# Performance work log

Measured on AMD Instinct MI355X. Metric: run time of the kernel, lower is better.

## Reference

```python
import jax, jax.numpy as jnp
import numpy as np

N_ATOMS = 100000
N_EDGES = 300000
ATOM_DIM = 32
BOND_DIM = 16
STEPS = 4


def setup_inputs() -> dict:
    key = jax.random.key(0)
    ks = jax.random.split(key, 8)
    atom_features = jax.random.normal(ks[0], (N_ATOMS, ATOM_DIM), dtype=jnp.float32)
    bond_features = jax.random.normal(ks[1], (N_EDGES, BOND_DIM), dtype=jnp.float32)
    pair_indices = jax.random.randint(ks[2], (N_EDGES, 2), 0, N_ATOMS, dtype=jnp.int64 if jax.config.jax_enable_x64 else jnp.int32)
    W_bond = jax.random.normal(ks[3], (BOND_DIM, ATOM_DIM * ATOM_DIM), dtype=jnp.float32) * 0.05
    b_bond = jnp.zeros((ATOM_DIM * ATOM_DIM,), dtype=jnp.float32)
    W_ih = jax.random.normal(ks[4], (3 * ATOM_DIM, ATOM_DIM), dtype=jnp.float32) * 0.1
    W_hh = jax.random.normal(ks[5], (3 * ATOM_DIM, ATOM_DIM), dtype=jnp.float32) * 0.1
    b_ih = jnp.zeros((3 * ATOM_DIM,), dtype=jnp.float32)
    b_hh = jnp.zeros((3 * ATOM_DIM,), dtype=jnp.float32)
    return {
        'atom_features': atom_features,
        'bond_features': bond_features,
        'pair_indices': pair_indices,
        'W_bond': W_bond, 'b_bond': b_bond,
        'W_ih': W_ih, 'W_hh': W_hh, 'b_ih': b_ih, 'b_hh': b_hh,
    }


def _gru_cell(x, h, W_ih, W_hh, b_ih, b_hh):
    # torch.nn.GRUCell semantics
    gi = x @ W_ih.T + b_ih  # [N, 3H]
    gh = h @ W_hh.T + b_hh
    i_r, i_z, i_n = jnp.split(gi, 3, axis=-1)
    h_r, h_z, h_n = jnp.split(gh, 3, axis=-1)
    r = jax.nn.sigmoid(i_r + h_r)
    z = jax.nn.sigmoid(i_z + h_z)
    n = jnp.tanh(i_n + r * h_n)
    return (1.0 - z) * n + z * h


def reference(atom_features, bond_features, pair_indices, W_bond, b_bond, W_ih, W_hh, b_ih, b_hh):
    n_atoms, d = atom_features.shape
    # Edge transform matrices (identical every step in the original; hoisted)
    edge_mats = (bond_features @ W_bond + b_bond).reshape(-1, d, d)  # [E, d, d]
    dst = pair_indices[:, 0]
    nbr = pair_indices[:, 1]
    h = atom_features
    for _ in range(STEPS):
        # gather neighbor states, per-edge matvec, scatter-add
        msg = jnp.einsum('eij,ej->ei', edge_mats, h[nbr])  # [E, d]
        agg = jax.ops.segment_sum(msg, dst, num_segments=n_atoms)  # [N, d]
        h = _gru_cell(agg, h, W_ih, W_hh, b_ih, b_hh)
    return h
```

## Files before the change

kernel.cpp:

```cpp
#include <hip/hip_runtime.h>
#include <hip/hip_cooperative_groups.h>

namespace cg = cooperative_groups;

#define NA 100000
#define NE 300000
#define STEPS 4
#define NTILES (NE / 16)
#define ATILES (NA / 16)

typedef _Float16 f16;
typedef _Float16 half8 __attribute__((ext_vector_type(8)));
using f32x4 = __attribute__((ext_vector_type(4))) float;

__global__ __launch_bounds__(256) void setup_kernel(
    const float* __restrict__ atom,
    const float* __restrict__ Wb, const float* __restrict__ bb,
    const float* __restrict__ Wih, const float* __restrict__ Whh,
    f16* __restrict__ hbf, f16* __restrict__ Wbt,
    f16* __restrict__ Wihb, f16* __restrict__ Whhb,
    int* __restrict__ rowcnt, int* __restrict__ total)
{
    int t = blockIdx.x * 256 + threadIdx.x;
    const int NH8 = NA * 32 / 8;
    if (t < NH8) {
        float4 a = reinterpret_cast<const float4*>(atom)[2 * t];
        float4 b = reinterpret_cast<const float4*>(atom)[2 * t + 1];
        half8 o;
        o[0]=(f16)a.x; o[1]=(f16)a.y; o[2]=(f16)a.z; o[3]=(f16)a.w;
        o[4]=(f16)b.x; o[5]=(f16)b.y; o[6]=(f16)b.z; o[7]=(f16)b.w;
        reinterpret_cast<half8*>(hbf)[t] = o;
        return;
    }
    int u = t - NH8;
    if (u < NA) {
        rowcnt[u] = 0;
        if (u == 0) *total = 0;
        return;
    }
    int v = u - NA;
    if (v < 17 * 32 * 32) {
        int j = v & 31, i = (v >> 5) & 31, k = v >> 10;
        float val = (k < 16) ? Wb[k * 1024 + i * 32 + j] : bb[i * 32 + j];
        int row = ((i & 4) ? 16 : 0) + ((i >> 3) << 2) + (i & 3);
        Wbt[(k * 32 + row) * 32 + j] = (f16)val;
    } else if (v < 17 * 32 * 32 + 3072) {
        int q = v - 17 * 32 * 32;
        Wihb[q] = (f16)Wih[q];
    } else if (v < 17 * 32 * 32 + 6144) {
        int q = v - 17 * 32 * 32 - 3072;
        Whhb[q] = (f16)Whh[q];
    }
}

__global__ __launch_bounds__(256) void hist_kernel(
    const int* __restrict__ pair, int* __restrict__ cnt)
{
    int e = blockIdx.x * 256 + threadIdx.x;
    if (e < NE) atomicAdd(&cnt[reinterpret_cast<const int2*>(pair)[e].x], 1);
}

__global__ __launch_bounds__(1024) void alloc_kernel(
    const int* __restrict__ cnt, int* __restrict__ start,
    int* __restrict__ next, int* __restrict__ total)
{
    __shared__ int tmp[1024];
    __shared__ int base;
    int g = blockIdx.x * 1024 + threadIdx.x;
    int v = (g < NA) ? cnt[g] : 0;
    tmp[threadIdx.x] = v;
    __syncthreads();
    for (int off = 1; off < 1024; off <<= 1) {
        int u = (threadIdx.x >= off) ? tmp[threadIdx.x - off] : 0;
        __syncthreads();
        tmp[threadIdx.x] += u;
        __syncthreads();
    }
    if (threadIdx.x == 1023) base = atomicAdd(total, tmp[1023]);
    __syncthreads();
    if (g < NA) {
        int s = base + tmp[threadIdx.x] - v;
        start[g] = s;
        next[g] = s;
    }
}

__global__ __launch_bounds__(256) void scatter_kernel(
    const float* __restrict__ bond, const int* __restrict__ pair,
    int* __restrict__ next, int* __restrict__ nbrp, f16* __restrict__ bondp)
{
    int e = blockIdx.x * 256 + threadIdx.x;
    if (e >= NE) return;
    int2 p = reinterpret_cast<const int2*>(pair)[e];
    int pos = atomicAdd(&next[p.x], 1);
    nbrp[pos] = p.y;
    const float4* b4 = reinterpret_cast<const float4*>(bond + (size_t)e * 16);
    float4 b0 = b4[0], b1 = b4[1], b2 = b4[2], b3 = b4[3];
    half8 o0, o1;
    o0[0]=(f16)b0.x; o0[1]=(f16)b0.y; o0[2]=(f16)b0.z; o0[3]=(f16)b0.w;
    o0[4]=(f16)b1.x; o0[5]=(f16)b1.y; o0[6]=(f16)b1.z; o0[7]=(f16)b1.w;
    o1[0]=(f16)b2.x; o1[1]=(f16)b2.y; o1[2]=(f16)b2.z; o1[3]=(f16)b2.w;
    o1[4]=(f16)b3.x; o1[5]=(f16)b3.y; o1[6]=(f16)b3.z; o1[7]=(f16)b3.w;
    half8* dst = reinterpret_cast<half8*>(bondp + (size_t)pos * 16);
    dst[0] = o0; dst[1] = o1;
}

__device__ __forceinline__ void msg_body(
    const f16* __restrict__ h, const f16* __restrict__ bondp,
    const int* __restrict__ nbrp, const f16* __restrict__ Wbt,
    f16* __restrict__ msgb, int wid, int nw, int col, int kg)
{
    half8 w0[17], w1[17];
#pragma unroll
    for (int t = 0; t < 17; ++t) {
        w0[t] = *reinterpret_cast<const half8*>(Wbt + (t * 32 + col) * 32 + kg * 8);
        w1[t] = *reinterpret_cast<const half8*>(Wbt + (t * 32 + 16 + col) * 32 + kg * 8);
    }
    int tile = wid;
    int pos = 0;
    half8 hf{}, cA{}, cB{};
    if (tile < NTILES) {
        pos = tile * 16 + col;
        int nbr0 = nbrp[pos];
        cA = *reinterpret_cast<const half8*>(bondp + (size_t)pos * 16);
        cB = *reinterpret_cast<const half8*>(bondp + (size_t)pos * 16 + 8);
        hf = *reinterpret_cast<const half8*>(h + (size_t)nbr0 * 32 + kg * 8);
    }
    while (tile < NTILES) {
        int tile2 = tile + nw;
        int pos2 = 0;
        half8 hf2{}, cA2{}, cB2{};
        if (tile2 < NTILES) {
            pos2 = tile2 * 16 + col;
            int nbr2 = nbrp[pos2];
            cA2 = *reinterpret_cast<const half8*>(bondp + (size_t)pos2 * 16);
            cB2 = *reinterpret_cast<const half8*>(bondp + (size_t)pos2 * 16 + 8);
            hf2 = *reinterpret_cast<const half8*>(h + (size_t)nbr2 * 32 + kg * 8);
        }
        f32x4 acc0 = {0.f, 0.f, 0.f, 0.f};
        f32x4 acc1 = {0.f, 0.f, 0.f, 0.f};
#pragma unroll
        for (int t = 0; t < 16; ++t) {
            f16 ch = (t < 8) ? cA[t] : cB[t - 8];
            half8 a = hf * ch;
            acc0 = __builtin_amdgcn_mfma_f32_16x16x32_f16(w0[t], a, acc0, 0, 0, 0);
            acc1 = __builtin_amdgcn_mfma_f32_16x16x32_f16(w1[t], a, acc1, 0, 0, 0);
        }
        acc0 = __builtin_amdgcn_mfma_f32_16x16x32_f16(w0[16], hf, acc0, 0, 0, 0);
        acc1 = __builtin_amdgcn_mfma_f32_16x16x32_f16(w1[16], hf, acc1, 0, 0, 0);

        half8 so;
        so[0]=(f16)acc0[0]; so[1]=(f16)acc0[1]; so[2]=(f16)acc0[2]; so[3]=(f16)acc0[3];
        so[4]=(f16)acc1[0]; so[5]=(f16)acc1[1]; so[6]=(f16)acc1[2]; so[7]=(f16)acc1[3];
        *reinterpret_cast<half8*>(msgb + (size_t)pos * 32 + kg * 8) = so;

        tile = tile2; pos = pos2; hf = hf2; cA = cA2; cB = cB2;
    }
}

__device__ __forceinline__ void gru_body(
    const f16* __restrict__ msgb, const int* __restrict__ start,
    const int* __restrict__ cnt, f16* __restrict__ h,
    const f16* __restrict__ Wihb, const f16* __restrict__ Whhb,
    const float* __restrict__ bih, const float* __restrict__ bhh,
    float* __restrict__ hout, int wf, int wid, int nw, int col, int kg)
{
    half8 wi[6], wh[6];
#pragma unroll
    for (int t = 0; t < 6; ++t) {
        wi[t] = *reinterpret_cast<const half8*>(Wihb + (size_t)(t * 16 + col) * 32 + kg * 8);
        wh[t] = *reinterpret_cast<const half8*>(Whhb + (size_t)(t * 16 + col) * 32 + kg * 8);
    }
    float br0  = bih[col]      + bhh[col];
    float bz0  = bih[32 + col] + bhh[32 + col];
    float bin0 = bih[64 + col];
    float bhn0 = bhh[64 + col];
    float br1  = bih[16 + col] + bhh[16 + col];
    float bz1  = bih[48 + col] + bhh[48 + col];
    float bin1 = bih[80 + col];
    float bhn1 = bhh[80 + col];

    for (int tile = wid; tile < ATILES; tile += nw) {
        int base = tile * 16;
        int a0   = base + col;
        int st = start[a0], en = st + cnt[a0];
        half8 hfrag = *reinterpret_cast<const half8*>(h + (size_t)a0 * 32 + kg * 8);

        float xs[8] = {0.f, 0.f, 0.f, 0.f, 0.f, 0.f, 0.f, 0.f};
        int p = st;
        while (p < en) {
            int n = en - p;
            half8 m0, m1, m2, m3;
            m0 = *reinterpret_cast<const half8*>(msgb + (size_t)p * 32 + kg * 8);
            if (n > 1) m1 = *reinterpret_cast<const half8*>(msgb + (size_t)(p + 1) * 32 + kg * 8);
            if (n > 2) m2 = *reinterpret_cast<const half8*>(msgb + (size_t)(p + 2) * 32 + kg * 8);
            if (n > 3) m3 = *reinterpret_cast<const half8*>(msgb + (size_t)(p + 3) * 32 + kg * 8);
#pragma unroll
            for (int j = 0; j < 8; ++j) xs[j] += (float)m0[j];
            if (n > 1) {
#pragma unroll
                for (int j = 0; j < 8; ++j) xs[j] += (float)m1[j];
            }
            if (n > 2) {
#pragma unroll
                for (int j = 0; j < 8; ++j) xs[j] += (float)m2[j];
            }
            if (n > 3) {
#pragma unroll
                for (int j = 0; j < 8; ++j) xs[j] += (float)m3[j];
            }
            p += 4;
        }
        half8 xfrag;
#pragma unroll
        for (int j = 0; j < 8; ++j) xfrag[j] = (f16)xs[j];

        f32x4 gi[6], gh[6];
#pragma unroll
        for (int t = 0; t < 6; ++t) {
            f32x4 z = {0.f, 0.f, 0.f, 0.f};
            gi[t] = __builtin_amdgcn_mfma_f32_16x16x32_f16(xfrag, wi[t], z, 0, 0, 0);
            gh[t] = __builtin_amdgcn_mfma_f32_16x16x32_f16(hfrag, wh[t], z, 0, 0, 0);
        }

#pragma unroll
        for (int hh = 0; hh < 2; ++hh) {
            float br  = hh ? br1  : br0;
            float bz  = hh ? bz1  : bz0;
            float bin = hh ? bin1 : bin0;
            float bhn = hh ? bhn1 : bhn0;
            int i = hh * 16 + col;
#pragma unroll
            for (int reg = 0; reg < 4; ++reg) {
                int a = base + kg * 4 + reg;
                float r = 1.f / (1.f + __expf(-(gi[hh][reg] + gh[hh][reg] + br)));
                float z = 1.f / (1.f + __expf(-(gi[2 + hh][reg] + gh[2 + hh][reg] + bz)));
                float n = tanhf(gi[4 + hh][reg] + bin + r * (gh[4 + hh][reg] + bhn));
                float hp = (float)h[(size_t)a * 32 + i];
                float o  = (1.f - z) * n + z * hp;
                if (wf) hout[(size_t)a * 32 + i] = o;
                h[(size_t)a * 32 + i] = (f16)o;
            }
        }
    }
}

__global__ __launch_bounds__(256, 2) void msg_kernel(
    const f16* __restrict__ hb, const f16* __restrict__ bondp,
    const int* __restrict__ nbrp, const f16* __restrict__ Wbt,
    f16* __restrict__ msgb)
{
    int wave = threadIdx.x >> 6;
    int lane = threadIdx.x & 63;
    msg_body(hb, bondp, nbrp, Wbt, msgb,
             blockIdx.x * 4 + wave, gridDim.x << 2, lane & 15, lane >> 4);
}

__global__ __launch_bounds__(256) void gru_kernel(
    const f16* __restrict__ msgb, const int* __restrict__ start,
    const int* __restrict__ cnt, f16* __restrict__ hb,
    const f16* __restrict__ Wihb, const f16* __restrict__ Whhb,
    const float* __restrict__ bih, const float* __restrict__ bhh,
    float* __restrict__ hout, int wf)
{
    int wave = threadIdx.x >> 6;
    int lane = threadIdx.x & 63;
    gru_body(msgb, start, cnt, hb, Wihb, Whhb, bih, bhh, hout, wf,
             blockIdx.x * 4 + wave, gridDim.x << 2, lane & 15, lane >> 4);
}

__global__ __launch_bounds__(256, 2) void step_kernel(
    f16* __restrict__ h, const f16* __restrict__ bondp,
    const int* __restrict__ nbrp, const f16* __restrict__ Wbt,
    f16* __restrict__ msgb, const int* __restrict__ start,
    const int* __restrict__ cnt,
    const f16* __restrict__ Wihb, const f16* __restrict__ Whhb,
    const float* __restrict__ bih, const float* __restrict__ bhh,
    float* __restrict__ hout)
{
    cg::grid_group grid = cg::this_grid();
    int wave = threadIdx.x >> 6;
    int lane = threadIdx.x & 63;
    int col  = lane & 15;
    int kg   = lane >> 4;
    int wid  = blockIdx.x * 4 + wave;
    int nw   = gridDim.x << 2;

    for (int s = 0; s < STEPS; ++s) {
        msg_body(h, bondp, nbrp, Wbt, msgb, wid, nw, col, kg);
        grid.sync();
        gru_body(msgb, start, cnt, h, Wihb, Whhb, bih, bhh, hout,
                 (s == STEPS - 1) ? 1 : 0, wid, nw, col, kg);
        grid.sync();
    }
}

extern "C" void kernel_launch(void* const* d_in, const int* in_sizes, int n_in,
                              void* d_out, int out_size, void* d_ws, size_t ws_size,
                              hipStream_t stream)
{
    const float* atom = (const float*)d_in[0];
    const float* bond = (const float*)d_in[1];
    const int*   pair = (const int*)  d_in[2];
    const float* Wb   = (const float*)d_in[3];
    const float* bb   = (const float*)d_in[4];
    const float* W_ih = (const float*)d_in[5];
    const float* W_hh = (const float*)d_in[6];
    const float* b_ih = (const float*)d_in[7];
    const float* b_hh = (const float*)d_in[8];
    float* out = (float*)d_out;

    char* w = (char*)d_ws;
    f16* msg    = (f16*)w;
    f16* hbf    = (f16*)(w + 19200000);
    f16* bondp  = (f16*)(w + 25600000);
    f16* Wbt    = (f16*)(w + 35200000);
    f16* Wihb   = Wbt + 17 * 32 * 32;
    f16* Whhb   = Wihb + 96 * 32;
    int* rowcnt = (int*)(w + 35248000);
    int* startp = (int*)(w + 35648000);
    int* nextp  = (int*)(w + 36048000);
    int* nbrp   = (int*)(w + 36448000);
    int* total  = (int*)(w + 37648000);

    const int setup_threads = NA * 32 / 8 + NA + 17 * 32 * 32 + 6144;
    setup_kernel<<<(setup_threads + 255) / 256, 256, 0, stream>>>(
        atom, Wb, bb, W_ih, W_hh, hbf, Wbt, Wihb, Whhb, rowcnt, total);
    hist_kernel<<<(NE + 255) / 256, 256, 0, stream>>>(pair, rowcnt);
    alloc_kernel<<<(NA + 1023) / 1024, 1024, 0, stream>>>(rowcnt, startp, nextp, total);
    scatter_kernel<<<(NE + 255) / 256, 256, 0, stream>>>(bond, pair, nextp, nbrp, bondp);

    int bpc = 0;
    hipError_t qe = hipOccupancyMaxActiveBlocksPerMultiprocessor(
        &bpc, (const void*)step_kernel, 256, 0);
    if (qe == hipSuccess && bpc >= 2) {
        int nblk = bpc * 256;
        if (nblk > 2048) nblk = 2048;
        void* args[12];
        args[0]  = &hbf;   args[1]  = &bondp;  args[2]  = &nbrp;
        args[3]  = &Wbt;   args[4]  = &msg;    args[5]  = &startp;
        args[6]  = &rowcnt; args[7] = &Wihb;   args[8]  = &Whhb;
        args[9]  = (void*)&b_ih; args[10] = (void*)&b_hh; args[11] = &out;
        hipLaunchCooperativeKernel((void*)step_kernel, dim3(nblk), dim3(256),
                                   args, 0, stream);
    } else {
        const int gru_blocks = (ATILES + 3) / 4;
        for (int s = 0; s < STEPS; ++s) {
            msg_kernel<<<512, 256, 0, stream>>>(hbf, bondp, nbrp, Wbt, msg);
            gru_kernel<<<gru_blocks, 256, 0, stream>>>(msg, startp, rowcnt, hbf,
                                                       Wihb, Whhb, b_ih, b_hh, out,
                                                       (s == STEPS - 1) ? 1 : 0);
        }
    }
}
```

Baseline: 195.1 us.

## Fold setup, histogram, scan and scatter preprocessing into cooperative mega kernel

Moves the four preprocessing kernels (f16 conversion, degree histogram, prefix-scan allocation, CSR scatter) into the single cooperative kernel, separated by grid.sync barriers, ahead of the message/GRU steps. This removes four separate kernel launches and their inter-kernel gaps. In exchange it adds grid-wide barriers, and the scan now runs in 256-wide chunks with more atomics on the total counter. The preprocessing work is also spread over a smaller persistent grid than the original per-element launches used.

Result: no change. 194.8 us, median of 2 (-0.2%).

```diff
diff --git a/kernel.cpp b/kernel.cpp
--- a/kernel.cpp
+++ b/kernel.cpp
@@ -13,15 +13,154 @@
 typedef _Float16 half8 __attribute__((ext_vector_type(8)));
 using f32x4 = __attribute__((ext_vector_type(4))) float;
 
-__global__ __launch_bounds__(256) void setup_kernel(
-    const float* __restrict__ atom,
+__device__ __forceinline__ void msg_body(
+    const f16* __restrict__ h, const f16* __restrict__ bondp,
+    const int* __restrict__ nbrp, const f16* __restrict__ Wbt,
+    f16* __restrict__ msgb, int wid, int nw, int col, int kg)
+{
+    half8 w0[17], w1[17];
+#pragma unroll
+    for (int t = 0; t < 17; ++t) {
+        w0[t] = *reinterpret_cast<const half8*>(Wbt + (t * 32 + col) * 32 + kg * 8);
+        w1[t] = *reinterpret_cast<const half8*>(Wbt + (t * 32 + 16 + col) * 32 + kg * 8);
+    }
+    int tile = wid;
+    int pos = 0;
+    half8 hf{}, cA{}, cB{};
+    if (tile < NTILES) {
+        pos = tile * 16 + col;
+        int nbr0 = nbrp[pos];
+        cA = *reinterpret_cast<const half8*>(bondp + (size_t)pos * 16);
+        cB = *reinterpret_cast<const half8*>(bondp + (size_t)pos * 16 + 8);
+        hf = *reinterpret_cast<const half8*>(h + (size_t)nbr0 * 32 + kg * 8);
+    }
+    while (tile < NTILES) {
+        int tile2 = tile + nw;
+        int pos2 = 0;
+        half8 hf2{}, cA2{}, cB2{};
+        if (tile2 < NTILES) {
+            pos2 = tile2 * 16 + col;
+            int nbr2 = nbrp[pos2];
+            cA2 = *reinterpret_cast<const half8*>(bondp + (size_t)pos2 * 16);
+            cB2 = *reinterpret_cast<const half8*>(bondp + (size_t)pos2 * 16 + 8);
+            hf2 = *reinterpret_cast<const half8*>(h + (size_t)nbr2 * 32 + kg * 8);
+        }
+        f32x4 acc0 = {0.f, 0.f, 0.f, 0.f};
+        f32x4 acc1 = {0.f, 0.f, 0.f, 0.f};
+#pragma unroll
+        for (int t = 0; t < 16; ++t) {
+            f16 ch = (t < 8) ? cA[t] : cB[t - 8];
+            half8 a = hf * ch;
+            acc0 = __builtin_amdgcn_mfma_f32_16x16x32_f16(w0[t], a, acc0, 0, 0, 0);
+            acc1 = __builtin_amdgcn_mfma_f32_16x16x32_f16(w1[t], a, acc1, 0, 0, 0);
+        }
+        acc0 = __builtin_amdgcn_mfma_f32_16x16x32_f16(w0[16], hf, acc0, 0, 0, 0);
+        acc1 = __builtin_amdgcn_mfma_f32_16x16x32_f16(w1[16], hf, acc1, 0, 0, 0);
+
+        half8 so;
+        so[0]=(f16)acc0[0]; so[1]=(f16)acc0[1]; so[2]=(f16)acc0[2]; so[3]=(f16)acc0[3];
+        so[4]=(f16)acc1[0]; so[5]=(f16)acc1[1]; so[6]=(f16)acc1[2]; so[7]=(f16)acc1[3];
+        *reinterpret_cast<half8*>(msgb + (size_t)pos * 32 + kg * 8) = so;
+
+        tile = tile2; pos = pos2; hf = hf2; cA = cA2; cB = cB2;
+    }
+}
+
+__device__ __forceinline__ void gru_body(
+    const f16* __restrict__ msgb, const int* __restrict__ start,
+    const int* __restrict__ cnt, f16* __restrict__ h,
+    const f16* __restrict__ Wihb, const f16* __restrict__ Whhb,
+    const float* __restrict__ bih, const float* __restrict__ bhh,
+    float* __restrict__ hout, int wf, int wid, int nw, int col, int kg)
+{
+    half8 wi[6], wh[6];
+#pragma unroll
+    for (int t = 0; t < 6; ++t) {
+        wi[t] = *reinterpret_cast<const half8*>(Wihb + (size_t)(t * 16 + col) * 32 + kg * 8);
+        wh[t] = *reinterpret_cast<const half8*>(Whhb + (size_t)(t * 16 + col) * 32 + kg * 8);
+    }
+    float br0  = bih[col]      + bhh[col];
+    float bz0  = bih[32 + col] + bhh[32 + col];
+    float bin0 = bih[64 + col];
+    float bhn0 = bhh[64 + col];
+    float br1  = bih[16 + col] + bhh[16 + col];
+    float bz1  = bih[48 + col] + bhh[48 + col];
+    float bin1 = bih[80 + col];
+    float bhn1 = bhh[80 + col];
+
+    for (int tile = wid; tile < ATILES; tile += nw) {
+        int base = tile * 16;
+        int a0   = base + col;
+        int st = start[a0], en = st + cnt[a0];
+        half8 hfrag = *reinterpret_cast<const half8*>(h + (size_t)a0 * 32 + kg * 8);
+
+        float xs[8] = {0.f, 0.f, 0.f, 0.f, 0.f, 0.f, 0.f, 0.f};
+        int p = st;
+        while (p < en) {
+            int n = en - p;
+            half8 m0, m1, m2, m3;
+            m0 = *reinterpret_cast<const half8*>(msgb + (size_t)p * 32 + kg * 8);
+            if (n > 1) m1 = *reinterpret_cast<const half8*>(msgb + (size_t)(p + 1) * 32 + kg * 8);
+            if (n > 2) m2 = *reinterpret_cast<const half8*>(msgb + (size_t)(p + 2) * 32 + kg * 8);
+            if (n > 3) m3 = *reinterpret_cast<const half8*>(msgb + (size_t)(p + 3) * 32 + kg * 8);
+#pragma unroll
+            for (int j = 0; j < 8; ++j) xs[j] += (float)m0[j];
+            if (n > 1) {
+#pragma unroll
+                for (int j = 0; j < 8; ++j) xs[j] += (float)m1[j];
+            }
+            if (n > 2) {
+#pragma unroll
+                for (int j = 0; j < 8; ++j) xs[j] += (float)m2[j];
+            }
+            if (n > 3) {
+#pragma unroll
+                for (int j = 0; j < 8; ++j) xs[j] += (float)m3[j];
+            }
+            p += 4;
+        }
+        half8 xfrag;
+#pragma unroll
+        for (int j = 0; j < 8; ++j) xfrag[j] = (f16)xs[j];
+
+        f32x4 gi[6], gh[6];
+#pragma unroll
+        for (int t = 0; t < 6; ++t) {
+            f32x4 z = {0.f, 0.f, 0.f, 0.f};
+            gi[t] = __builtin_amdgcn_mfma_f32_16x16x32_f16(xfrag, wi[t], z, 0, 0, 0);
+            gh[t] = __builtin_amdgcn_mfma_f32_16x16x32_f16(hfrag, wh[t], z, 0, 0, 0);
+        }
+
+#pragma unroll
+        for (int hh = 0; hh < 2; ++hh) {
+            float br  = hh ? br1  : br0;
+            float bz  = hh ? bz1  : bz0;
+            float bin = hh ? bin1 : bin0;
+            float bhn = hh ? bhn1 : bhn0;
+            int i = hh * 16 + col;
+#pragma unroll
+            for (int reg = 0; reg < 4; ++reg) {
+                int a = base + kg * 4 + reg;
+                float r = 1.f / (1.f + __expf(-(gi[hh][reg] + gh[hh][reg] + br)));
+                float z = 1.f / (1.f + __expf(-(gi[2 + hh][reg] + gh[2 + hh][reg] + bz)));
+                float n = tanhf(gi[4 + hh][reg] + bin + r * (gh[4 + hh][reg] + bhn));
+                float hp = (float)h[(size_t)a * 32 + i];
+                float o  = (1.f - z) * n + z * hp;
+                if (wf) hout[(size_t)a * 32 + i] = o;
+                h[(size_t)a * 32 + i] = (f16)o;
+            }
+        }
+    }
+}
+
+__device__ __forceinline__ void setup_item(
+    int t, const float* __restrict__ atom,
     const float* __restrict__ Wb, const float* __restrict__ bb,
     const float* __restrict__ Wih, const float* __restrict__ Whh,
     f16* __restrict__ hbf, f16* __restrict__ Wbt,
     f16* __restrict__ Wihb, f16* __restrict__ Whhb,
     int* __restrict__ rowcnt, int* __restrict__ total)
 {
-    int t = blockIdx.x * 256 + threadIdx.x;
     const int NH8 = NA * 32 / 8;
     if (t < NH8) {
         float4 a = reinterpret_cast<const float4*>(atom)[2 * t];
@@ -53,44 +192,10 @@
     }
 }
 
-__global__ __launch_bounds__(256) void hist_kernel(
-    const int* __restrict__ pair, int* __restrict__ cnt)
-{
-    int e = blockIdx.x * 256 + threadIdx.x;
-    if (e < NE) atomicAdd(&cnt[reinterpret_cast<const int2*>(pair)[e].x], 1);
-}
-
-__global__ __launch_bounds__(1024) void alloc_kernel(
-    const int* __restrict__ cnt, int* __restrict__ start,
-    int* __restrict__ next, int* __restrict__ total)
-{
-    __shared__ int tmp[1024];
-    __shared__ int base;
-    int g = blockIdx.x * 1024 + threadIdx.x;
-    int v = (g < NA) ? cnt[g] : 0;
-    tmp[threadIdx.x] = v;
-    __syncthreads();
-    for (int off = 1; off < 1024; off <<= 1) {
-        int u = (threadIdx.x >= off) ? tmp[threadIdx.x - off] : 0;
-        __syncthreads();
-        tmp[threadIdx.x] += u;
-        __syncthreads();
-    }
-    if (threadIdx.x == 1023) base = atomicAdd(total, tmp[1023]);
-    __syncthreads();
-    if (g < NA) {
-        int s = base + tmp[threadIdx.x] - v;
-        start[g] = s;
-        next[g] = s;
-    }
-}
-
-__global__ __launch_bounds__(256) void scatter_kernel(
-    const float* __restrict__ bond, const int* __restrict__ pair,
+__device__ __forceinline__ void scatter_item(
+    int e, const float* __restrict__ bond, const int* __restrict__ pair,
     int* __restrict__ next, int* __restrict__ nbrp, f16* __restrict__ bondp)
 {
-    int e = blockIdx.x * 256 + threadIdx.x;
-    if (e >= NE) return;
     int2 p = reinterpret_cast<const int2*>(pair)[e];
     int pos = atomicAdd(&next[p.x], 1);
     nbrp[pos] = p.y;
@@ -105,144 +210,130 @@
     dst[0] = o0; dst[1] = o1;
 }
 
-__device__ __forceinline__ void msg_body(
-    const f16* __restrict__ h, const f16* __restrict__ bondp,
-    const int* __restrict__ nbrp, const f16* __restrict__ Wbt,
-    f16* __restrict__ msgb, int wid, int nw, int col, int kg)
-{
-    half8 w0[17], w1[17];
-#pragma unroll
-    for (int t = 0; t < 17; ++t) {
-        w0[t] = *reinterpret_cast<const half8*>(Wbt + (t * 32 + col) * 32 + kg * 8);
-        w1[t] = *reinterpret_cast<const half8*>(Wbt + (t * 32 + 16 + col) * 32 + kg * 8);
-    }
-    int tile = wid;
-    int pos = 0;
-    half8 hf{}, cA{}, cB{};
-    if (tile < NTILES) {
-        pos = tile * 16 + col;
-        int nbr0 = nbrp[pos];
-        cA = *reinterpret_cast<const half8*>(bondp + (size_t)pos * 16);
-        cB = *reinterpret_cast<const half8*>(bondp + (size_t)pos * 16 + 8);
-        hf = *reinterpret_cast<const half8*>(h + (size_t)nbr0 * 32 + kg * 8);
-    }
-    while (tile < NTILES) {
-        int tile2 = tile + nw;
-        int pos2 = 0;
-        half8 hf2{}, cA2{}, cB2{};
-        if (tile2 < NTILES) {
-            pos2 = tile2 * 16 + col;
-            int nbr2 = nbrp[pos2];
-            cA2 = *reinterpret_cast<const half8*>(bondp + (size_t)pos2 * 16);
-            cB2 = *reinterpret_cast<const half8*>(bondp + (size_t)pos2 * 16 + 8);
-            hf2 = *reinterpret_cast<const half8*>(h + (size_t)nbr2 * 32 + kg * 8);
-        }
-        f32x4 acc0 = {0.f, 0.f, 0.f, 0.f};
-        f32x4 acc1 = {0.f, 0.f, 0.f, 0.f};
-#pragma unroll
-        for (int t = 0; t < 16; ++t) {
-            f16 ch = (t < 8) ? cA[t] : cB[t - 8];
-            half8 a = hf * ch;
-            acc0 = __builtin_amdgcn_mfma_f32_16x16x32_f16(w0[t], a, acc0, 0, 0, 0);
-            acc1 = __builtin_amdgcn_mfma_f32_16x16x32_f16(w1[t], a, acc1, 0, 0, 0);
-        }
-        acc0 = __builtin_amdgcn_mfma_f32_16x16x32_f16(w0[16], hf, acc0, 0, 0, 0);
-        acc1 = __builtin_amdgcn_mfma_f32_16x16x32_f16(w1[16], hf, acc1, 0, 0, 0);
-
-        half8 so;
-        so[0]=(f16)acc0[0]; so[1]=(f16)acc0[1]; so[2]=(f16)acc0[2]; so[3]=(f16)acc0[3];
-        so[4]=(f16)acc1[0]; so[5]=(f16)acc1[1]; so[6]=(f16)acc1[2]; so[7]=(f16)acc1[3];
-        *reinterpret_cast<half8*>(msgb + (size_t)pos * 32 + kg * 8) = so;
-
-        tile = tile2; pos = pos2; hf = hf2; cA = cA2; cB = cB2;
-    }
-}
-
-__device__ __forceinline__ void gru_body(
-    const f16* __restrict__ msgb, const int* __restrict__ start,
-    const int* __restrict__ cnt, f16* __restrict__ h,
-    const f16* __restrict__ Wihb, const f16* __restrict__ Whhb,
+#define SETUP_THREADS (NA * 32 / 8 + NA + 17 * 32 * 32 + 6144)
+
+__global__ __launch_bounds__(256, 2) void mega_kernel(
+    const float* __restrict__ atom, const float* __restrict__ bond,
+    const int* __restrict__ pair,
+    const float* __restrict__ Wb, const float* __restrict__ bb,
+    const float* __restrict__ Wih, const float* __restrict__ Whh,
     const float* __restrict__ bih, const float* __restrict__ bhh,
-    float* __restrict__ hout, int wf, int wid, int nw, int col, int kg)
-{
-    half8 wi[6], wh[6];
-#pragma unroll
-    for (int t = 0; t < 6; ++t) {
-        wi[t] = *reinterpret_cast<const half8*>(Wihb + (size_t)(t * 16 + col) * 32 + kg * 8);
-        wh[t] = *reinterpret_cast<const half8*>(Whhb + (size_t)(t * 16 + col) * 32 + kg * 8);
-    }
-    float br0  = bih[col]      + bhh[col];
-    float bz0  = bih[32 + col] + bhh[32 + col];
-    float bin0 = bih[64 + col];
-    float bhn0 = bhh[64 + col];
-    float br1  = bih[16 + col] + bhh[16 + col];
-    float bz1  = bih[48 + col] + bhh[48 + col];
-    float bin1 = bih[80 + col];
-    float bhn1 = bhh[80 + col];
-
-    for (int tile = wid; tile < ATILES; tile += nw) {
-        int base = tile * 16;
-        int a0   = base + col;
-        int st = start[a0], en = st + cnt[a0];
-        half8 hfrag = *reinterpret_cast<const half8*>(h + (size_t)a0 * 32 + kg * 8);
-
-        float xs[8] = {0.f, 0.f, 0.f, 0.f, 0.f, 0.f, 0.f, 0.f};
-        int p = st;
-        while (p < en) {
-            int n = en - p;
-            half8 m0, m1, m2, m3;
-            m0 = *reinterpret_cast<const half8*>(msgb + (size_t)p * 32 + kg * 8);
-            if (n > 1) m1 = *reinterpret_cast<const half8*>(msgb + (size_t)(p + 1) * 32 + kg * 8);
-            if (n > 2) m2 = *reinterpret_cast<const half8*>(msgb + (size_t)(p + 2) * 32 + kg * 8);
-            if (n > 3) m3 = *reinterpret_cast<const half8*>(msgb + (size_t)(p + 3) * 32 + kg * 8);
-#pragma unroll
-            for (int j = 0; j < 8; ++j) xs[j] += (float)m0[j];
-            if (n > 1) {
-#pragma unroll
-                for (int j = 0; j < 8; ++j) xs[j] += (float)m1[j];
-            }
-            if (n > 2) {
-#pragma unroll
-                for (int j = 0; j < 8; ++j) xs[j] += (float)m2[j];
-            }
-            if (n > 3) {
-#pragma unroll
-                for (int j = 0; j < 8; ++j) xs[j] += (float)m3[j];
-            }
-            p += 4;
-        }
-        half8 xfrag;
-#pragma unroll
-        for (int j = 0; j < 8; ++j) xfrag[j] = (f16)xs[j];
-
-        f32x4 gi[6], gh[6];
-#pragma unroll
-        for (int t = 0; t < 6; ++t) {
-            f32x4 z = {0.f, 0.f, 0.f, 0.f};
-            gi[t] = __builtin_amdgcn_mfma_f32_16x16x32_f16(xfrag, wi[t], z, 0, 0, 0);
-            gh[t] = __builtin_amdgcn_mfma_f32_16x16x32_f16(hfrag, wh[t], z, 0, 0, 0);
-        }
-
-#pragma unroll
-        for (int hh = 0; hh < 2; ++hh) {
-            float br  = hh ? br1  : br0;
-            float bz  = hh ? bz1  : bz0;
-            float bin = hh ? bin1 : bin0;
-            float bhn = hh ? bhn1 : bhn0;
-            int i = hh * 16 + col;
-#pragma unroll
-            for (int reg = 0; reg < 4; ++reg) {
-                int a = base + kg * 4 + reg;
-                float r = 1.f / (1.f + __expf(-(gi[hh][reg] + gh[hh][reg] + br)));
-                float z = 1.f / (1.f + __expf(-(gi[2 + hh][reg] + gh[2 + hh][reg] + bz)));
-                float n = tanhf(gi[4 + hh][reg] + bin + r * (gh[4 + hh][reg] + bhn));
-                float hp = (float)h[(size_t)a * 32 + i];
-                float o  = (1.f - z) * n + z * hp;
-                if (wf) hout[(size_t)a * 32 + i] = o;
-                h[(size_t)a * 32 + i] = (f16)o;
-            }
-        }
-    }
+    f16* __restrict__ hbf, f16* __restrict__ Wbt,
+    f16* __restrict__ Wihb, f16* __restrict__ Whhb,
+    int* __restrict__ rowcnt, int* __restrict__ startp, int* __restrict__ nextp,
+    int* __restrict__ nbrp, f16* __restrict__ bondp,
+    f16* __restrict__ msgb, int* __restrict__ total,
+    float* __restrict__ hout)
+{
+    __shared__ int scan[256];
+    __shared__ int sbase;
+
+    cg::grid_group grid = cg::this_grid();
+    int gtid = blockIdx.x * 256 + threadIdx.x;
+    int gsz  = gridDim.x * 256;
+
+    for (int t = gtid; t < SETUP_THREADS; t += gsz)
+        setup_item(t, atom, Wb, bb, Wih, Whh, hbf, Wbt, Wihb, Whhb, rowcnt, total);
+    grid.sync();
+
+    for (int e = gtid; e < NE; e += gsz)
+        atomicAdd(&rowcnt[reinterpret_cast<const int2*>(pair)[e].x], 1);
+    grid.sync();
+
+    const int NCHUNK = (NA + 255) / 256;
+    for (int chunk = blockIdx.x; chunk < NCHUNK; chunk += gridDim.x) {
+        int g = chunk * 256 + threadIdx.x;
+        int v = (g < NA) ? rowcnt[g] : 0;
+        scan[threadIdx.x] = v;
+        __syncthreads();
+        for (int off = 1; off < 256; off <<= 1) {
+            int u = (threadIdx.x >= off) ? scan[threadIdx.x - off] : 0;
+            __syncthreads();
+            scan[threadIdx.x] += u;
+            __syncthreads();
+        }
+        if (threadIdx.x == 255) sbase = atomicAdd(total, scan[255]);
+        __syncthreads();
+        if (g < NA) {
+            int s = sbase + scan[threadIdx.x] - v;
+            startp[g] = s;
+            nextp[g]  = s;
+        }
+        __syncthreads();
+    }
+    grid.sync();
+
+    for (int e = gtid; e < NE; e += gsz)
+        scatter_item(e, bond, pair, nextp, nbrp, bondp);
+    grid.sync();
+
+    int wave = threadIdx.x >> 6;
+    int lane = threadIdx.x & 63;
+    int col  = lane & 15;
+    int kg   = lane >> 4;
+    int wid  = blockIdx.x * 4 + wave;
+    int nw   = gridDim.x << 2;
+
+    for (int s = 0; s < STEPS; ++s) {
+        msg_body(hbf, bondp, nbrp, Wbt, msgb, wid, nw, col, kg);
+        grid.sync();
+        gru_body(msgb, startp, rowcnt, hbf, Wihb, Whhb, bih, bhh, hout,
+                 (s == STEPS - 1) ? 1 : 0, wid, nw, col, kg);
+        grid.sync();
+    }
+}
+
+__global__ __launch_bounds__(256) void setup_kernel(
+    const float* __restrict__ atom,
+    const float* __restrict__ Wb, const float* __restrict__ bb,
+    const float* __restrict__ Wih, const float* __restrict__ Whh,
+    f16* __restrict__ hbf, f16* __restrict__ Wbt,
+    f16* __restrict__ Wihb, f16* __restrict__ Whhb,
+    int* __restrict__ rowcnt, int* __restrict__ total)
+{
+    int t = blockIdx.x * 256 + threadIdx.x;
+    if (t < SETUP_THREADS)
+        setup_item(t, atom, Wb, bb, Wih, Whh, hbf, Wbt, Wihb, Whhb, rowcnt, total);
+}
+
+__global__ __launch_bounds__(256) void hist_kernel(
+    const int* __restrict__ pair, int* __restrict__ cnt)
+{
+    int e = blockIdx.x * 256 + threadIdx.x;
+    if (e < NE) atomicAdd(&cnt[reinterpret_cast<const int2*>(pair)[e].x], 1);
+}
+
+__global__ __launch_bounds__(1024) void alloc_kernel(
+    const int* __restrict__ cnt, int* __restrict__ start,
+    int* __restrict__ next, int* __restrict__ total)
+{
+    __shared__ int tmp[1024];
+    __shared__ int base;
+    int g = blockIdx.x * 1024 + threadIdx.x;
+    int v = (g < NA) ? cnt[g] : 0;
+    tmp[threadIdx.x] = v;
+    __syncthreads();
+    for (int off = 1; off < 1024; off <<= 1) {
+        int u = (threadIdx.x >= off) ? tmp[threadIdx.x - off] : 0;
+        __syncthreads();
+        tmp[threadIdx.x] += u;
+        __syncthreads();
+    }
+    if (threadIdx.x == 1023) base = atomicAdd(total, tmp[1023]);
+    __syncthreads();
+    if (g < NA) {
+        int s = base + tmp[threadIdx.x] - v;
+        start[g] = s;
+        next[g] = s;
+    }
+}
+
+__global__ __launch_bounds__(256) void scatter_kernel(
+    const float* __restrict__ bond, const int* __restrict__ pair,
+    int* __restrict__ next, int* __restrict__ nbrp, f16* __restrict__ bondp)
+{
+    int e = blockIdx.x * 256 + threadIdx.x;
+    if (e < NE) scatter_item(e, bond, pair, next, nbrp, bondp);
 }
 
 __global__ __launch_bounds__(256, 2) void msg_kernel(
@@ -267,32 +358,6 @@
     int lane = threadIdx.x & 63;
     gru_body(msgb, start, cnt, hb, Wihb, Whhb, bih, bhh, hout, wf,
              blockIdx.x * 4 + wave, gridDim.x << 2, lane & 15, lane >> 4);
-}
-
-__global__ __launch_bounds__(256, 2) void step_kernel(
-    f16* __restrict__ h, const f16* __restrict__ bondp,
-    const int* __restrict__ nbrp, const f16* __restrict__ Wbt,
-    f16* __restrict__ msgb, const int* __restrict__ start,
-    const int* __restrict__ cnt,
-    const f16* __restrict__ Wihb, const f16* __restrict__ Whhb,
-    const float* __restrict__ bih, const float* __restrict__ bhh,
-    float* __restrict__ hout)
-{
-    cg::grid_group grid = cg::this_grid();
-    int wave = threadIdx.x >> 6;
-    int lane = threadIdx.x & 63;
-    int col  = lane & 15;
-    int kg   = lane >> 4;
-    int wid  = blockIdx.x * 4 + wave;
-    int nw   = gridDim.x << 2;
-
-    for (int s = 0; s < STEPS; ++s) {
-        msg_body(h, bondp, nbrp, Wbt, msgb, wid, nw, col, kg);
-        grid.sync();
-        gru_body(msgb, start, cnt, h, Wihb, Whhb, bih, bhh, hout,
-                 (s == STEPS - 1) ? 1 : 0, wid, nw, col, kg);
-        grid.sync();
-    }
 }
 
 extern "C" void kernel_launch(void* const* d_in, const int* in_sizes, int n_in,
@@ -323,27 +388,29 @@
     int* nbrp   = (int*)(w + 36448000);
     int* total  = (int*)(w + 37648000);
 
-    const int setup_threads = NA * 32 / 8 + NA + 17 * 32 * 32 + 6144;
-    setup_kernel<<<(setup_threads + 255) / 256, 256, 0, stream>>>(
-        atom, Wb, bb, W_ih, W_hh, hbf, Wbt, Wihb, Whhb, rowcnt, total);
-    hist_kernel<<<(NE + 255) / 256, 256, 0, stream>>>(pair, rowcnt);
-    alloc_kernel<<<(NA + 1023) / 1024, 1024, 0, stream>>>(rowcnt, startp, nextp, total);
-    scatter_kernel<<<(NE + 255) / 256, 256, 0, stream>>>(bond, pair, nextp, nbrp, bondp);
-
     int bpc = 0;
     hipError_t qe = hipOccupancyMaxActiveBlocksPerMultiprocessor(
-        &bpc, (const void*)step_kernel, 256, 0);
+        &bpc, (const void*)mega_kernel, 256, 0);
     if (qe == hipSuccess && bpc >= 2) {
         int nblk = bpc * 256;
         if (nblk > 2048) nblk = 2048;
-        void* args[12];
-        args[0]  = &hbf;   args[1]  = &bondp;  args[2]  = &nbrp;
-        args[3]  = &Wbt;   args[4]  = &msg;    args[5]  = &startp;
-        args[6]  = &rowcnt; args[7] = &Wihb;   args[8]  = &Whhb;
-        args[9]  = (void*)&b_ih; args[10] = (void*)&b_hh; args[11] = &out;
-        hipLaunchCooperativeKernel((void*)step_kernel, dim3(nblk), dim3(256),
+        void* args[21];
+        args[0]  = (void*)&atom;  args[1]  = (void*)&bond;  args[2]  = (void*)&pair;
+        args[3]  = (void*)&Wb;    args[4]  = (void*)&bb;
+        args[5]  = (void*)&W_ih;  args[6]  = (void*)&W_hh;
+        args[7]  = (void*)&b_ih;  args[8]  = (void*)&b_hh;
+        args[9]  = &hbf;   args[10] = &Wbt;   args[11] = &Wihb;  args[12] = &Whhb;
+        args[13] = &rowcnt; args[14] = &startp; args[15] = &nextp;
+        args[16] = &nbrp;  args[17] = &bondp; args[18] = &msg;
+        args[19] = &total; args[20] = &out;
+        hipLaunchCooperativeKernel((void*)mega_kernel, dim3(nblk), dim3(256),
                                    args, 0, stream);
     } else {
+        setup_kernel<<<(SETUP_THREADS + 255) / 256, 256, 0, stream>>>(
+            atom, Wb, bb, W_ih, W_hh, hbf, Wbt, Wihb, Whhb, rowcnt, total);
+        hist_kernel<<<(NE + 255) / 256, 256, 0, stream>>>(pair, rowcnt);
+        alloc_kernel<<<(NA + 1023) / 1024, 1024, 0, stream>>>(rowcnt, startp, nextp, total);
+        scatter_kernel<<<(NE + 255) / 256, 256, 0, stream>>>(bond, pair, nextp, nbrp, bondp);
         const int gru_blocks = (ATILES + 3) / 4;
         for (int s = 0; s < STEPS; ++s) {
             msg_kernel<<<512, 256, 0, stream>>>(hbf, bondp, nbrp, Wbt, msg);
```
